# Kernel optimization log

Measured on AMD Instinct MI355X. Metric: run time of the kernel, lower is better.

The kernel has to match this reference:

```python
import jax, jax.numpy as jnp
import numpy as np

NUM_NODES = 100000
IN_CH = 128
OUT_CH = 64
NUM_EDGES = 1000000


def setup_inputs() -> dict:
    key = jax.random.key(0)
    ks = jax.random.split(key, 16)

    x = jax.random.normal(ks[0], (NUM_NODES, IN_CH), dtype=jnp.float32)

    def make_edges(k_src, k_tgt, k_w):
        src = jax.random.randint(k_src, (NUM_EDGES,), 0, NUM_NODES, dtype=jnp.int32)
        # tf.math.segment_sum requires sorted segment ids -> sort targets
        tgt = jnp.sort(jax.random.randint(k_tgt, (NUM_EDGES,), 0, NUM_NODES, dtype=jnp.int32))
        ei = jnp.stack([src, tgt], axis=0)  # (2, E)
        ew = jax.random.uniform(k_w, (NUM_EDGES,), dtype=jnp.float32)
        return ei, ew

    edge_index_in, edge_weight_in = make_edges(ks[1], ks[2], ks[3])
    edge_index_out, edge_weight_out = make_edges(ks[4], ks[5], ks[6])

    glorot = (6.0 / (IN_CH + OUT_CH)) ** 0.5
    W_main_in = jax.random.uniform(ks[7], (IN_CH, OUT_CH), minval=-glorot, maxval=glorot, dtype=jnp.float32)
    W_main_out = jax.random.uniform(ks[8], (IN_CH, OUT_CH), minval=-glorot, maxval=glorot, dtype=jnp.float32)
    W_shared = jax.random.uniform(ks[9], (IN_CH, OUT_CH), minval=-glorot, maxval=glorot, dtype=jnp.float32)

    bias_main_in = jnp.zeros((OUT_CH,), dtype=jnp.float32)
    bias_main_out = jnp.zeros((OUT_CH,), dtype=jnp.float32)
    bias_shared_in = jnp.zeros((OUT_CH,), dtype=jnp.float32)
    bias_shared_out = jnp.zeros((OUT_CH,), dtype=jnp.float32)

    C_in_vec = jnp.ones((NUM_NODES, 1), dtype=jnp.float32)
    C_out_vec = jnp.ones((NUM_NODES, 1), dtype=jnp.float32)

    return {
        "x": x,
        "W_main_in": W_main_in,
        "W_main_out": W_main_out,
        "W_shared": W_shared,
        "bias_main_in": bias_main_in,
        "bias_main_out": bias_main_out,
        "bias_shared_in": bias_shared_in,
        "bias_shared_out": bias_shared_out,
        "C_in_vec": C_in_vec,
        "C_out_vec": C_out_vec,
        "edge_index_in": edge_index_in,
        "edge_weight_in": edge_weight_in,
        "edge_index_out": edge_index_out,
        "edge_weight_out": edge_weight_out,
    }


def _propagate(h, edge_index, edge_weight, num_nodes):
    # gather messages from source nodes, scale by edge weight, sum into targets
    src = edge_index[0]
    tgt = edge_index[1]
    msgs = h[src] * edge_weight[:, None]  # (E, OUT_CH)
    return jax.ops.segment_sum(msgs, tgt, num_segments=num_nodes)  # (N, OUT_CH)


def reference(x, W_main_in, W_main_out, W_shared,
              bias_main_in, bias_main_out, bias_shared_in, bias_shared_out,
              C_in_vec, C_out_vec,
              edge_index_in, edge_weight_in, edge_index_out, edge_weight_out):
    n = x.shape[0]
    h_main_in = _propagate(x @ W_main_in, edge_index_in, edge_weight_in, n)
    h_shared_in = _propagate(x @ W_shared, edge_index_in, edge_weight_in, n)
    ic_combined = h_main_in + bias_main_in + (h_shared_in + bias_shared_in)

    h_main_out = _propagate(x @ W_main_out, edge_index_out, edge_weight_out, n)
    h_shared_out = _propagate(x @ W_shared, edge_index_out, edge_weight_out, n)
    oc_combined = h_main_out + bias_main_out + (h_shared_out + bias_shared_out)

    return C_in_vec * ic_combined + C_out_vec * oc_combined
```

## Files before the change

kernel.cpp:

```cpp
#include <hip/hip_runtime.h>

#define IN_CH   128
#define OUT_CH  64
#define M_TILE  128
#define XS_PITCH 136

typedef __attribute__((ext_vector_type(8))) short short8;
typedef __attribute__((ext_vector_type(4))) float floatx4;

__device__ __forceinline__ unsigned short f2bf(float f) {
    union { float f; unsigned u; } v; v.f = f;
    unsigned r = v.u + 0x7fffu + ((v.u >> 16) & 1u);
    return (unsigned short)(r >> 16);
}
__device__ __forceinline__ float bfl(unsigned u) {
    return __uint_as_float(u << 16);
}
__device__ __forceinline__ float bfh(unsigned u) {
    return __uint_as_float(u & 0xffff0000u);
}

__global__ void prep_kernel(const int* __restrict__ tgtIn,
                            const int* __restrict__ tgtOut,
                            const float* __restrict__ Wmi,
                            const float* __restrict__ Wmo,
                            const float* __restrict__ Wsh,
                            int* __restrict__ rpIn,
                            int* __restrict__ rpOut,
                            unsigned short* __restrict__ WcT,
                            int n_nodes, int neIn, int neOut)
{
    int i = blockIdx.x * blockDim.x + threadIdx.x;
    int half = n_nodes + 1;
    if (i < 2 * half) {
        const int* tgt; int* rp; int t; int ne;
        if (i < half) { tgt = tgtIn;  rp = rpIn;  t = i;        ne = neIn; }
        else          { tgt = tgtOut; rp = rpOut; t = i - half; ne = neOut; }
        int lo = 0, hi = ne;
        while (lo < hi) {
            int mid = (lo + hi) >> 1;
            if (tgt[mid] < t) lo = mid + 1; else hi = mid;
        }
        rp[t] = lo;
    } else {
        int j = i - 2 * half;
        if (j < 2 * OUT_CH * IN_CH) {
            int n = j >> 7, k = j & 127;
            float m = (n < OUT_CH) ? Wmi[k * OUT_CH + n]
                                   : Wmo[k * OUT_CH + (n - OUT_CH)];
            float s = Wsh[k * OUT_CH + (n & (OUT_CH - 1))];
            WcT[n * IN_CH + k] = f2bf(m + s);
        }
    }
}

__global__ __launch_bounds__(256, 3)
void gemm_kernel(const float* __restrict__ x,
                 const unsigned short* __restrict__ WcT,
                 unsigned short* __restrict__ Abf,
                 unsigned short* __restrict__ Bbf,
                 int n_nodes)
{
    __shared__ unsigned short Xs[M_TILE][XS_PITCH];

    const int tid  = threadIdx.x;
    const int w    = tid >> 6;
    const int lane = tid & 63;
    const int l15  = lane & 15;
    const int quad = lane >> 4;
    const long long node0 = (long long)blockIdx.x * M_TILE;

    short8 bfrag[4][2];
#pragma unroll
    for (int ks = 0; ks < 4; ++ks)
#pragma unroll
        for (int ni = 0; ni < 2; ++ni)
            bfrag[ks][ni] = *(const short8*)&WcT[(w * 32 + ni * 16 + l15) * IN_CH
                                                 + ks * 32 + quad * 8];

    {
        const float4* x4 = (const float4*)x;
        for (int i = tid; i < M_TILE * (IN_CH / 4); i += 256) {
            int row = i >> 5, c4 = i & 31;
            long long node = node0 + row;
            float4 v = make_float4(0.f, 0.f, 0.f, 0.f);
            if (node < n_nodes) v = x4[node * (IN_CH / 4) + c4];
            uint2 p;
            p.x = ((unsigned)f2bf(v.y) << 16) | f2bf(v.x);
            p.y = ((unsigned)f2bf(v.w) << 16) | f2bf(v.z);
            *(uint2*)&Xs[row][c4 * 4] = p;
        }
    }
    __syncthreads();

    floatx4 acc[8][2];
#pragma unroll
    for (int mi = 0; mi < 8; ++mi)
#pragma unroll
        for (int ni = 0; ni < 2; ++ni)
            acc[mi][ni] = (floatx4){0.f, 0.f, 0.f, 0.f};

#pragma unroll
    for (int ks = 0; ks < 4; ++ks) {
        const int k0 = ks * 32 + quad * 8;
#pragma unroll
        for (int mi = 0; mi < 8; ++mi) {
            short8 a = *(const short8*)&Xs[mi * 16 + l15][k0];
            acc[mi][0] = __builtin_amdgcn_mfma_f32_16x16x32_bf16(a, bfrag[ks][0], acc[mi][0], 0, 0, 0);
            acc[mi][1] = __builtin_amdgcn_mfma_f32_16x16x32_bf16(a, bfrag[ks][1], acc[mi][1], 0, 0, 0);
        }
    }

    unsigned short* Hout = (w < 2) ? Abf : Bbf;
    const int colb = (w & 1) * 32;
#pragma unroll
    for (int mi = 0; mi < 8; ++mi)
#pragma unroll
        for (int ni = 0; ni < 2; ++ni)
#pragma unroll
            for (int r = 0; r < 4; ++r) {
                long long row = node0 + mi * 16 + quad * 4 + r;
                if (row < n_nodes)
                    Hout[row * OUT_CH + colb + ni * 16 + l15] = f2bf(acc[mi][ni][r]);
            }
}

__global__ __launch_bounds__(256)
void prop_kernel(const unsigned short* __restrict__ H,
                 const int* __restrict__ rpIn, const int* __restrict__ rpOut,
                 const int* __restrict__ srcIn, const float* __restrict__ ewIn,
                 const int* __restrict__ srcOut, const float* __restrict__ ewOut,
                 const float* __restrict__ bmi, const float* __restrict__ bmo,
                 const float* __restrict__ bsi, const float* __restrict__ bso,
                 const float* __restrict__ Cin, const float* __restrict__ Cout,
                 float* __restrict__ out, int n_nodes, int neIn, int neOut)
{
    const int lane = threadIdx.x & 63;
    const int wv   = threadIdx.x >> 6;
    const int e    = lane >> 3;
    const int el   = lane & 7;
    const int ch8  = el * 8;
    const int eb   = lane & 56;

    const unsigned short* Hq = H + ch8;

    const int t = ((int)blockIdx.x * 4 + wv) * 8 + e;
    const bool valid = (t < n_nodes);
    const int tc = valid ? t : 0;

    const int Boff = n_nodes * OUT_CH;

    int ei0 = rpIn[tc],  ei1 = rpIn[tc + 1];
    int eo0 = rpOut[tc], eo1 = rpOut[tc + 1];
    int dIn  = ei1 - ei0;
    int len  = valid ? (dIn + (eo1 - eo0)) : 0;
    float ci = Cin[tc], co = Cout[tc];

    int ml = len;
    ml = max(ml, __shfl_xor(ml, 8));
    ml = max(ml, __shfl_xor(ml, 16));
    ml = max(ml, __shfl_xor(ml, 32));
    const int maxlen = __builtin_amdgcn_readfirstlane(ml);

    float a0 = 0.f, a1 = 0.f, a2 = 0.f, a3 = 0.f;
    float a4 = 0.f, a5 = 0.f, a6 = 0.f, a7 = 0.f;

    auto load_raw = [&](int j, int& sI, float& wI, int& sO, float& wO) {
        int iIn  = min(ei0 + max(0, min(j, dIn - 1)), neIn - 1);
        int jo   = j - dIn;
        int iOut = min(eo0 + max(0, jo), neOut - 1);
        sI = srcIn[iIn];  wI = ewIn[iIn];
        sO = srcOut[iOut]; wO = ewOut[iOut];
    };

    auto conv = [&](int p, int sI, float wI, int sO, float wO,
                    int& rowb, float& wj) {
        int j = p + el;
        bool inSeg  = (j < dIn);
        bool anySeg = (j < len);
        int rb = inSeg ? (sI * OUT_CH) : (sO * OUT_CH + Boff);
        rowb = anySeg ? rb : 0;
        wj   = inSeg ? (ci * wI) : (anySeg ? (co * wO) : 0.f);
    };

    auto gather = [&](int rowb, uint4 (&u)[8]) {
        int r0 = __shfl(rowb, eb + 0), r1 = __shfl(rowb, eb + 1);
        int r2 = __shfl(rowb, eb + 2), r3 = __shfl(rowb, eb + 3);
        int r4 = __shfl(rowb, eb + 4), r5 = __shfl(rowb, eb + 5);
        int r6 = __shfl(rowb, eb + 6), r7 = __shfl(rowb, eb + 7);
        u[0] = *(const uint4*)(Hq + r0);
        u[1] = *(const uint4*)(Hq + r1);
        u[2] = *(const uint4*)(Hq + r2);
        u[3] = *(const uint4*)(Hq + r3);
        u[4] = *(const uint4*)(Hq + r4);
        u[5] = *(const uint4*)(Hq + r5);
        u[6] = *(const uint4*)(Hq + r6);
        u[7] = *(const uint4*)(Hq + r7);
    };

    auto consume = [&](const uint4 (&u)[8], float wj) {
#pragma unroll
        for (int k = 0; k < 8; ++k) {
            float wk = __shfl(wj, eb + k);
            uint4 uk = u[k];
            a0 += wk * bfl(uk.x); a1 += wk * bfh(uk.x);
            a2 += wk * bfl(uk.y); a3 += wk * bfh(uk.y);
            a4 += wk * bfl(uk.z); a5 += wk * bfh(uk.z);
            a6 += wk * bfl(uk.w); a7 += wk * bfh(uk.w);
        }
    };

    int   sIa, sOa, sIb, sOb;
    float wIa, wOa, wIb, wOb;
    uint4 uA[8], uB[8];
    float wjA = 0.f, wjB = 0.f;

    load_raw(el,     sIa, wIa, sOa, wOa);
    load_raw(8 + el, sIb, wIb, sOb, wOb);
    {
        int rb; conv(0, sIa, wIa, sOa, wOa, rb, wjA);
        gather(rb, uA);
    }
    load_raw(16 + el, sIa, wIa, sOa, wOa);
    {
        int rb; conv(8, sIb, wIb, sOb, wOb, rb, wjB);
        gather(rb, uB);
    }
    load_raw(24 + el, sIb, wIb, sOb, wOb);

    for (int p = 0; p < maxlen; p += 16) {
        consume(uA, wjA);
        if (p + 16 < maxlen) {
            int rb; conv(p + 16, sIa, wIa, sOa, wOa, rb, wjA);
            load_raw(p + 32 + el, sIa, wIa, sOa, wOa);
            gather(rb, uA);
        }
        if (p + 8 < maxlen) consume(uB, wjB);
        if (p + 24 < maxlen) {
            int rb; conv(p + 24, sIb, wIb, sOb, wOb, rb, wjB);
            load_raw(p + 40 + el, sIb, wIb, sOb, wOb);
            gather(rb, uB);
        }
    }

    if (valid) {
        float4 o0, o1;
        o0.x = a0 + ci * (bmi[ch8 + 0] + bsi[ch8 + 0]) + co * (bmo[ch8 + 0] + bso[ch8 + 0]);
        o0.y = a1 + ci * (bmi[ch8 + 1] + bsi[ch8 + 1]) + co * (bmo[ch8 + 1] + bso[ch8 + 1]);
        o0.z = a2 + ci * (bmi[ch8 + 2] + bsi[ch8 + 2]) + co * (bmo[ch8 + 2] + bso[ch8 + 2]);
        o0.w = a3 + ci * (bmi[ch8 + 3] + bsi[ch8 + 3]) + co * (bmo[ch8 + 3] + bso[ch8 + 3]);
        o1.x = a4 + ci * (bmi[ch8 + 4] + bsi[ch8 + 4]) + co * (bmo[ch8 + 4] + bso[ch8 + 4]);
        o1.y = a5 + ci * (bmi[ch8 + 5] + bsi[ch8 + 5]) + co * (bmo[ch8 + 5] + bso[ch8 + 5]);
        o1.z = a6 + ci * (bmi[ch8 + 6] + bsi[ch8 + 6]) + co * (bmo[ch8 + 6] + bso[ch8 + 6]);
        o1.w = a7 + ci * (bmi[ch8 + 7] + bsi[ch8 + 7]) + co * (bmo[ch8 + 7] + bso[ch8 + 7]);
        float* ob = out + (long long)t * OUT_CH + ch8;
        *(float4*)ob = o0;
        *(float4*)(ob + 4) = o1;
    }
}

extern "C" void kernel_launch(void* const* d_in, const int* in_sizes, int n_in,
                              void* d_out, int out_size, void* d_ws, size_t ws_size,
                              hipStream_t stream)
{
    const float* x    = (const float*)d_in[0];
    const float* Wmi  = (const float*)d_in[1];
    const float* Wmo  = (const float*)d_in[2];
    const float* Wsh  = (const float*)d_in[3];
    const float* bmi  = (const float*)d_in[4];
    const float* bmo  = (const float*)d_in[5];
    const float* bsi  = (const float*)d_in[6];
    const float* bso  = (const float*)d_in[7];
    const float* Cin  = (const float*)d_in[8];
    const float* Cout = (const float*)d_in[9];
    const int*   eiIn  = (const int*)d_in[10];
    const float* ewIn  = (const float*)d_in[11];
    const int*   eiOut = (const int*)d_in[12];
    const float* ewOut = (const float*)d_in[13];

    const int n_nodes = in_sizes[0] / IN_CH;
    const int neIn  = in_sizes[11];
    const int neOut = in_sizes[13];

    const int* srcIn  = eiIn;
    const int* tgtIn  = eiIn + neIn;
    const int* srcOut = eiOut;
    const int* tgtOut = eiOut + neOut;

    char* ws = (char*)d_ws;
    size_t NH = (size_t)n_nodes * OUT_CH * sizeof(unsigned short);
    unsigned short* Abf = (unsigned short*)ws;
    unsigned short* Bbf = (unsigned short*)(ws + NH);
    int* rpIn  = (int*)(ws + 2 * NH);
    int* rpOut = rpIn + (n_nodes + 1);
    unsigned short* WcT = (unsigned short*)(rpOut + (n_nodes + 1));

    int prep_threads = 2 * (n_nodes + 1) + 2 * OUT_CH * IN_CH;
    prep_kernel<<<(prep_threads + 255) / 256, 256, 0, stream>>>(
        tgtIn, tgtOut, Wmi, Wmo, Wsh, rpIn, rpOut, WcT, n_nodes, neIn, neOut);

    int gblocks = (n_nodes + M_TILE - 1) / M_TILE;
    gemm_kernel<<<gblocks, 256, 0, stream>>>(x, WcT, Abf, Bbf, n_nodes);

    int pblocks = (n_nodes + 31) / 32;
    prop_kernel<<<pblocks, 256, 0, stream>>>(
        Abf, rpIn, rpOut, srcIn, ewIn, srcOut, ewOut,
        bmi, bmo, bsi, bso, Cin, Cout, (float*)d_out, n_nodes, neIn, neOut);
}
```

Measured before the change: 184.9 us.

## Switch propagation to edge-parallel blocks with shared-memory atomic accumulation

Each block of the propagation kernel now owns a range of 64 target nodes. Its waves stride over that range's edge list in groups of 64 edges. Messages that share a target within each 8-edge group are pre-summed in registers, then added with LDS atomics into a shared per-block accumulator, and bias and C-scaling are applied at writeback. This removes the per-wave padding to the longest degree among 8 nodes, which degree variance made costly. In exchange it adds LDS atomic traffic, a target-index load per edge, and block-level syncs.

Result: slower. 318.7 us (+72.3%).

```diff
diff --git a/kernel.cpp b/kernel.cpp
--- a/kernel.cpp
+++ b/kernel.cpp
@@ -4,6 +4,9 @@
 #define OUT_CH  64
 #define M_TILE  128
 #define XS_PITCH 136
+
+#define NB         64
+#define ACC_STRIDE 68
 
 typedef __attribute__((ext_vector_type(8))) short short8;
 typedef __attribute__((ext_vector_type(4))) float floatx4;
@@ -129,133 +132,152 @@
 void prop_kernel(const unsigned short* __restrict__ H,
                  const int* __restrict__ rpIn, const int* __restrict__ rpOut,
                  const int* __restrict__ srcIn, const float* __restrict__ ewIn,
+                 const int* __restrict__ tgtIn,
                  const int* __restrict__ srcOut, const float* __restrict__ ewOut,
+                 const int* __restrict__ tgtOut,
                  const float* __restrict__ bmi, const float* __restrict__ bmo,
                  const float* __restrict__ bsi, const float* __restrict__ bso,
                  const float* __restrict__ Cin, const float* __restrict__ Cout,
                  float* __restrict__ out, int n_nodes, int neIn, int neOut)
 {
-    const int lane = threadIdx.x & 63;
-    const int wv   = threadIdx.x >> 6;
+    __shared__ float accL[NB * ACC_STRIDE];
+    __shared__ float CinL[NB], CoutL[NB];
+    __shared__ float bInL[OUT_CH], bOutL[OUT_CH];
+
+    const int tid  = threadIdx.x;
+    const int base = (int)blockIdx.x * NB;
+    const int nb   = min(NB, n_nodes - base);
+
+    for (int i = tid; i < NB * ACC_STRIDE; i += 256) accL[i] = 0.f;
+    if (tid < NB) {
+        int node = base + min(tid, nb - 1);
+        CinL[tid]  = Cin[node];
+        CoutL[tid] = Cout[node];
+    } else if (tid < NB + OUT_CH) {
+        int c = tid - NB;
+        bInL[c]  = bmi[c] + bsi[c];
+        bOutL[c] = bmo[c] + bso[c];
+    }
+    __syncthreads();
+
+    const int lane = tid & 63;
+    const int wv   = tid >> 6;
     const int e    = lane >> 3;
     const int el   = lane & 7;
     const int ch8  = el * 8;
     const int eb   = lane & 56;
 
-    const unsigned short* Hq = H + ch8;
-
-    const int t = ((int)blockIdx.x * 4 + wv) * 8 + e;
-    const bool valid = (t < n_nodes);
-    const int tc = valid ? t : 0;
+    float* accP = accL + ch8;
 
     const int Boff = n_nodes * OUT_CH;
 
-    int ei0 = rpIn[tc],  ei1 = rpIn[tc + 1];
-    int eo0 = rpOut[tc], eo1 = rpOut[tc + 1];
-    int dIn  = ei1 - ei0;
-    int len  = valid ? (dIn + (eo1 - eo0)) : 0;
-    float ci = Cin[tc], co = Cout[tc];
-
-    int ml = len;
-    ml = max(ml, __shfl_xor(ml, 8));
-    ml = max(ml, __shfl_xor(ml, 16));
-    ml = max(ml, __shfl_xor(ml, 32));
-    const int maxlen = __builtin_amdgcn_readfirstlane(ml);
-
-    float a0 = 0.f, a1 = 0.f, a2 = 0.f, a3 = 0.f;
-    float a4 = 0.f, a5 = 0.f, a6 = 0.f, a7 = 0.f;
-
-    auto load_raw = [&](int j, int& sI, float& wI, int& sO, float& wO) {
-        int iIn  = min(ei0 + max(0, min(j, dIn - 1)), neIn - 1);
-        int jo   = j - dIn;
-        int iOut = min(eo0 + max(0, jo), neOut - 1);
-        sI = srcIn[iIn];  wI = ewIn[iIn];
-        sO = srcOut[iOut]; wO = ewOut[iOut];
+    auto run_set = [&](const int* __restrict__ srcS, const float* __restrict__ ewS,
+                       const int* __restrict__ tgtS, int i0, int i1,
+                       const float* __restrict__ CL, const unsigned short* __restrict__ Hs)
+    {
+        const int ein = i1 - i0;
+        if (ein <= 0) return;
+        const unsigned short* Hq = Hs + ch8;
+        const int NPK = (ein + 63) >> 6;
+
+        auto mvalid = [&](int m) { return (wv + 4 * m) < NPK; };
+
+        auto loadE = [&](int m, int& s, float& w, int& t) {
+            int g   = (wv + 4 * m) * 64 + e * 8 + el;
+            int idx = i0 + min(g, ein - 1);
+            s = srcS[idx]; w = ewS[idx]; t = tgtS[idx];
+            if (g >= ein) w = 0.f;
+        };
+
+        auto prep = [&](int s, float w, int t, int& tl, float& wj, uint4 (&u)[8]) {
+            tl = t - base;
+            wj = w * CL[tl];
+#pragma unroll
+            for (int k = 0; k < 8; ++k) {
+                int sk = __shfl(s, eb + k);
+                u[k] = *(const uint4*)(Hq + sk * OUT_CH);
+            }
+        };
+
+        auto merge = [&](int tl, float wj, const uint4 (&u)[8]) {
+            int cur = __shfl(tl, eb);
+            float s0 = 0.f, s1 = 0.f, s2 = 0.f, s3 = 0.f;
+            float s4 = 0.f, s5 = 0.f, s6 = 0.f, s7 = 0.f;
+#pragma unroll
+            for (int k = 0; k < 8; ++k) {
+                int   tk = __shfl(tl, eb + k);
+                float wk = __shfl(wj, eb + k);
+                if (tk != cur) {
+                    float* p = accP + cur * ACC_STRIDE;
+                    atomicAdd(p + 0, s0); atomicAdd(p + 1, s1);
+                    atomicAdd(p + 2, s2); atomicAdd(p + 3, s3);
+                    atomicAdd(p + 4, s4); atomicAdd(p + 5, s5);
+                    atomicAdd(p + 6, s6); atomicAdd(p + 7, s7);
+                    s0 = s1 = s2 = s3 = s4 = s5 = s6 = s7 = 0.f;
+                    cur = tk;
+                }
+                uint4 uk = u[k];
+                s0 += wk * bfl(uk.x); s1 += wk * bfh(uk.x);
+                s2 += wk * bfl(uk.y); s3 += wk * bfh(uk.y);
+                s4 += wk * bfl(uk.z); s5 += wk * bfh(uk.z);
+                s6 += wk * bfl(uk.w); s7 += wk * bfh(uk.w);
+            }
+            float* p = accP + cur * ACC_STRIDE;
+            atomicAdd(p + 0, s0); atomicAdd(p + 1, s1);
+            atomicAdd(p + 2, s2); atomicAdd(p + 3, s3);
+            atomicAdd(p + 4, s4); atomicAdd(p + 5, s5);
+            atomicAdd(p + 6, s6); atomicAdd(p + 7, s7);
+        };
+
+        if (!mvalid(0)) return;
+
+        int   sA, tA; float wA;
+        int   sB, tB; float wB;
+        int   tlA, tlB; float wjA, wjB;
+        uint4 uA[8], uB[8];
+
+        loadE(0, sA, wA, tA);
+        const bool v1 = mvalid(1);
+        if (v1) loadE(1, sB, wB, tB);
+        prep(sA, wA, tA, tlA, wjA, uA);
+        if (mvalid(2)) loadE(2, sA, wA, tA);
+        if (v1) {
+            prep(sB, wB, tB, tlB, wjB, uB);
+            if (mvalid(3)) loadE(3, sB, wB, tB);
+        }
+
+        for (int m = 0; mvalid(m); m += 2) {
+            merge(tlA, wjA, uA);
+            if (mvalid(m + 2)) {
+                prep(sA, wA, tA, tlA, wjA, uA);
+                if (mvalid(m + 4)) loadE(m + 4, sA, wA, tA);
+            }
+            if (mvalid(m + 1)) {
+                merge(tlB, wjB, uB);
+                if (mvalid(m + 3)) {
+                    prep(sB, wB, tB, tlB, wjB, uB);
+                    if (mvalid(m + 5)) loadE(m + 5, sB, wB, tB);
+                }
+            }
+        }
     };
 
-    auto conv = [&](int p, int sI, float wI, int sO, float wO,
-                    int& rowb, float& wj) {
-        int j = p + el;
-        bool inSeg  = (j < dIn);
-        bool anySeg = (j < len);
-        int rb = inSeg ? (sI * OUT_CH) : (sO * OUT_CH + Boff);
-        rowb = anySeg ? rb : 0;
-        wj   = inSeg ? (ci * wI) : (anySeg ? (co * wO) : 0.f);
-    };
-
-    auto gather = [&](int rowb, uint4 (&u)[8]) {
-        int r0 = __shfl(rowb, eb + 0), r1 = __shfl(rowb, eb + 1);
-        int r2 = __shfl(rowb, eb + 2), r3 = __shfl(rowb, eb + 3);
-        int r4 = __shfl(rowb, eb + 4), r5 = __shfl(rowb, eb + 5);
-        int r6 = __shfl(rowb, eb + 6), r7 = __shfl(rowb, eb + 7);
-        u[0] = *(const uint4*)(Hq + r0);
-        u[1] = *(const uint4*)(Hq + r1);
-        u[2] = *(const uint4*)(Hq + r2);
-        u[3] = *(const uint4*)(Hq + r3);
-        u[4] = *(const uint4*)(Hq + r4);
-        u[5] = *(const uint4*)(Hq + r5);
-        u[6] = *(const uint4*)(Hq + r6);
-        u[7] = *(const uint4*)(Hq + r7);
-    };
-
-    auto consume = [&](const uint4 (&u)[8], float wj) {
-#pragma unroll
-        for (int k = 0; k < 8; ++k) {
-            float wk = __shfl(wj, eb + k);
-            uint4 uk = u[k];
-            a0 += wk * bfl(uk.x); a1 += wk * bfh(uk.x);
-            a2 += wk * bfl(uk.y); a3 += wk * bfh(uk.y);
-            a4 += wk * bfl(uk.z); a5 += wk * bfh(uk.z);
-            a6 += wk * bfl(uk.w); a7 += wk * bfh(uk.w);
-        }
-    };
-
-    int   sIa, sOa, sIb, sOb;
-    float wIa, wOa, wIb, wOb;
-    uint4 uA[8], uB[8];
-    float wjA = 0.f, wjB = 0.f;
-
-    load_raw(el,     sIa, wIa, sOa, wOa);
-    load_raw(8 + el, sIb, wIb, sOb, wOb);
-    {
-        int rb; conv(0, sIa, wIa, sOa, wOa, rb, wjA);
-        gather(rb, uA);
-    }
-    load_raw(16 + el, sIa, wIa, sOa, wOa);
-    {
-        int rb; conv(8, sIb, wIb, sOb, wOb, rb, wjB);
-        gather(rb, uB);
-    }
-    load_raw(24 + el, sIb, wIb, sOb, wOb);
-
-    for (int p = 0; p < maxlen; p += 16) {
-        consume(uA, wjA);
-        if (p + 16 < maxlen) {
-            int rb; conv(p + 16, sIa, wIa, sOa, wOa, rb, wjA);
-            load_raw(p + 32 + el, sIa, wIa, sOa, wOa);
-            gather(rb, uA);
-        }
-        if (p + 8 < maxlen) consume(uB, wjB);
-        if (p + 24 < maxlen) {
-            int rb; conv(p + 24, sIb, wIb, sOb, wOb, rb, wjB);
-            load_raw(p + 40 + el, sIb, wIb, sOb, wOb);
-            gather(rb, uB);
-        }
-    }
-
-    if (valid) {
-        float4 o0, o1;
-        o0.x = a0 + ci * (bmi[ch8 + 0] + bsi[ch8 + 0]) + co * (bmo[ch8 + 0] + bso[ch8 + 0]);
-        o0.y = a1 + ci * (bmi[ch8 + 1] + bsi[ch8 + 1]) + co * (bmo[ch8 + 1] + bso[ch8 + 1]);
-        o0.z = a2 + ci * (bmi[ch8 + 2] + bsi[ch8 + 2]) + co * (bmo[ch8 + 2] + bso[ch8 + 2]);
-        o0.w = a3 + ci * (bmi[ch8 + 3] + bsi[ch8 + 3]) + co * (bmo[ch8 + 3] + bso[ch8 + 3]);
-        o1.x = a4 + ci * (bmi[ch8 + 4] + bsi[ch8 + 4]) + co * (bmo[ch8 + 4] + bso[ch8 + 4]);
-        o1.y = a5 + ci * (bmi[ch8 + 5] + bsi[ch8 + 5]) + co * (bmo[ch8 + 5] + bso[ch8 + 5]);
-        o1.z = a6 + ci * (bmi[ch8 + 6] + bsi[ch8 + 6]) + co * (bmo[ch8 + 6] + bso[ch8 + 6]);
-        o1.w = a7 + ci * (bmi[ch8 + 7] + bsi[ch8 + 7]) + co * (bmo[ch8 + 7] + bso[ch8 + 7]);
-        float* ob = out + (long long)t * OUT_CH + ch8;
-        *(float4*)ob = o0;
-        *(float4*)(ob + 4) = o1;
+    run_set(srcIn,  ewIn,  tgtIn,  rpIn[base],  rpIn[base + nb],  CinL,  H);
+    run_set(srcOut, ewOut, tgtOut, rpOut[base], rpOut[base + nb], CoutL, H + Boff);
+
+    __syncthreads();
+
+    for (int j = tid; j < nb * 16; j += 256) {
+        int i = j >> 4;
+        int q = (j & 15) * 4;
+        float ci = CinL[i], co = CoutL[i];
+        const float* ar = accL + i * ACC_STRIDE + q;
+        float4 v;
+        v.x = ar[0] + ci * bInL[q + 0] + co * bOutL[q + 0];
+        v.y = ar[1] + ci * bInL[q + 1] + co * bOutL[q + 1];
+        v.z = ar[2] + ci * bInL[q + 2] + co * bOutL[q + 2];
+        v.w = ar[3] + ci * bInL[q + 3] + co * bOutL[q + 3];
+        *(float4*)(out + (long long)(base + i) * OUT_CH + q) = v;
     }
 }
 
@@ -302,8 +324,8 @@
     int gblocks = (n_nodes + M_TILE - 1) / M_TILE;
     gemm_kernel<<<gblocks, 256, 0, stream>>>(x, WcT, Abf, Bbf, n_nodes);
 
-    int pblocks = (n_nodes + 31) / 32;
+    int pblocks = (n_nodes + NB - 1) / NB;
     prop_kernel<<<pblocks, 256, 0, stream>>>(
-        Abf, rpIn, rpOut, srcIn, ewIn, srcOut, ewOut,
+        Abf, rpIn, rpOut, srcIn, ewIn, tgtIn, srcOut, ewOut, tgtOut,
         bmi, bmo, bsi, bso, Cin, Cout, (float*)d_out, n_nodes, neIn, neOut);
 }
```

## Sort nodes by degree within blocks and stage GEMM output through LDS

Applied to the files above, without the earlier changes.

Adds a kernel that bitonic-sorts each group of 256 nodes by combined in/out degree and writes a permutation. The propagation kernel uses it so the 8 nodes sharing a wavefront have similar edge counts, which cuts divergence from the per-wave maximum length loop. The GEMM epilogue now writes bf16 results into shared memory and then stores them as coalesced 16-byte vectors instead of scattered 2-byte stores. Costs are an extra kernel launch, an extra indirection, and output writes in permuted row order, which may hurt coalescing.

Measured after the change: 205.6 us. +11.2%, slower.

```diff
diff --git a/kernel.cpp b/kernel.cpp
--- a/kernel.cpp
+++ b/kernel.cpp
@@ -52,6 +52,36 @@
             WcT[n * IN_CH + k] = f2bf(m + s);
         }
     }
+}
+
+__global__ __launch_bounds__(256)
+void wsort_kernel(const int* __restrict__ rpIn, const int* __restrict__ rpOut,
+                  int* __restrict__ perm, int n_nodes)
+{
+    __shared__ unsigned key[256];
+    const int tid  = threadIdx.x;
+    const int base = (int)blockIdx.x * 256;
+    const int t    = base + tid;
+
+    int d = 0x7FFF;
+    if (t < n_nodes)
+        d = min((rpIn[t + 1] - rpIn[t]) + (rpOut[t + 1] - rpOut[t]), 0x7FFE);
+    key[tid] = ((unsigned)d << 16) | (unsigned)tid;
+
+    for (int k = 2; k <= 256; k <<= 1) {
+        for (int j = k >> 1; j > 0; j >>= 1) {
+            __syncthreads();
+            int ixj = tid ^ j;
+            if (ixj > tid) {
+                unsigned a = key[tid], b = key[ixj];
+                bool asc = (tid & k) == 0;
+                if (asc ? (a > b) : (a < b)) { key[tid] = b; key[ixj] = a; }
+            }
+        }
+    }
+    __syncthreads();
+    if (t < n_nodes)
+        perm[t] = base + (int)(key[tid] & 0xFFFFu);
 }
 
 __global__ __launch_bounds__(256, 3)
@@ -111,18 +141,29 @@
         }
     }
 
-    unsigned short* Hout = (w < 2) ? Abf : Bbf;
-    const int colb = (w & 1) * 32;
+    __syncthreads();
+    const int colb = w * 32;
 #pragma unroll
     for (int mi = 0; mi < 8; ++mi)
 #pragma unroll
         for (int ni = 0; ni < 2; ++ni)
 #pragma unroll
-            for (int r = 0; r < 4; ++r) {
-                long long row = node0 + mi * 16 + quad * 4 + r;
-                if (row < n_nodes)
-                    Hout[row * OUT_CH + colb + ni * 16 + l15] = f2bf(acc[mi][ni][r]);
-            }
+            for (int r = 0; r < 4; ++r)
+                Xs[mi * 16 + quad * 4 + r][colb + ni * 16 + l15] =
+                    f2bf(acc[mi][ni][r]);
+    __syncthreads();
+
+    for (int i = tid; i < M_TILE * 16; i += 256) {
+        int row  = i >> 4;
+        int half = (i >> 3) & 1;
+        int v4   = i & 7;
+        long long node = node0 + row;
+        if (node < n_nodes) {
+            uint4 v = *(const uint4*)&Xs[row][half * 64 + v4 * 8];
+            unsigned short* dst = half ? Bbf : Abf;
+            *(uint4*)&dst[node * OUT_CH + v4 * 8] = v;
+        }
+    }
 }
 
 __global__ __launch_bounds__(256)
@@ -130,6 +171,7 @@
                  const int* __restrict__ rpIn, const int* __restrict__ rpOut,
                  const int* __restrict__ srcIn, const float* __restrict__ ewIn,
                  const int* __restrict__ srcOut, const float* __restrict__ ewOut,
+                 const int* __restrict__ perm,
                  const float* __restrict__ bmi, const float* __restrict__ bmo,
                  const float* __restrict__ bsi, const float* __restrict__ bso,
                  const float* __restrict__ Cin, const float* __restrict__ Cout,
@@ -146,7 +188,7 @@
 
     const int t = ((int)blockIdx.x * 4 + wv) * 8 + e;
     const bool valid = (t < n_nodes);
-    const int tc = valid ? t : 0;
+    const int tc = valid ? perm[t] : 0;
 
     const int Boff = n_nodes * OUT_CH;
 
@@ -253,7 +295,7 @@
         o1.y = a5 + ci * (bmi[ch8 + 5] + bsi[ch8 + 5]) + co * (bmo[ch8 + 5] + bso[ch8 + 5]);
         o1.z = a6 + ci * (bmi[ch8 + 6] + bsi[ch8 + 6]) + co * (bmo[ch8 + 6] + bso[ch8 + 6]);
         o1.w = a7 + ci * (bmi[ch8 + 7] + bsi[ch8 + 7]) + co * (bmo[ch8 + 7] + bso[ch8 + 7]);
-        float* ob = out + (long long)t * OUT_CH + ch8;
+        float* ob = out + (long long)tc * OUT_CH + ch8;
         *(float4*)ob = o0;
         *(float4*)(ob + 4) = o1;
     }
@@ -294,16 +336,20 @@
     int* rpIn  = (int*)(ws + 2 * NH);
     int* rpOut = rpIn + (n_nodes + 1);
     unsigned short* WcT = (unsigned short*)(rpOut + (n_nodes + 1));
+    int* perm = (int*)(WcT + 2 * OUT_CH * IN_CH);
 
     int prep_threads = 2 * (n_nodes + 1) + 2 * OUT_CH * IN_CH;
     prep_kernel<<<(prep_threads + 255) / 256, 256, 0, stream>>>(
         tgtIn, tgtOut, Wmi, Wmo, Wsh, rpIn, rpOut, WcT, n_nodes, neIn, neOut);
 
+    int wblocks = (n_nodes + 255) / 256;
+    wsort_kernel<<<wblocks, 256, 0, stream>>>(rpIn, rpOut, perm, n_nodes);
+
     int gblocks = (n_nodes + M_TILE - 1) / M_TILE;
     gemm_kernel<<<gblocks, 256, 0, stream>>>(x, WcT, Abf, Bbf, n_nodes);
 
     int pblocks = (n_nodes + 31) / 32;
     prop_kernel<<<pblocks, 256, 0, stream>>>(
-        Abf, rpIn, rpOut, srcIn, ewIn, srcOut, ewOut,
+        Abf, rpIn, rpOut, srcIn, ewIn, srcOut, ewOut, perm,
         bmi, bmo, bsi, bso, Cin, Cout, (float*)d_out, n_nodes, neIn, neOut);
 }
```

## Build CSR row pointers per edge and stage GEMM output through LDS

Applied to the files above, without the earlier changes.

Row-pointer construction switches from a per-node binary search over sorted targets to a per-edge boundary scan, where each edge writes the row pointers between its predecessor's target and its own. This replaces roughly twenty dependent global reads per node with two coalesced reads per edge. The GEMM epilogue now writes bf16 accumulators into the shared X tile and then issues coalesced 16-byte stores to the two H buffers, instead of scattered 2-byte stores. The cost is two extra barriers, and the prep kernel launches more threads (one per edge rather than one per node).

Measured after the change: 182.3 us. Within noise of the previous version (-1.4%).

```diff
diff --git a/kernel.cpp b/kernel.cpp
--- a/kernel.cpp
+++ b/kernel.cpp
@@ -31,19 +31,22 @@
                             int n_nodes, int neIn, int neOut)
 {
     int i = blockIdx.x * blockDim.x + threadIdx.x;
-    int half = n_nodes + 1;
-    if (i < 2 * half) {
-        const int* tgt; int* rp; int t; int ne;
-        if (i < half) { tgt = tgtIn;  rp = rpIn;  t = i;        ne = neIn; }
-        else          { tgt = tgtOut; rp = rpOut; t = i - half; ne = neOut; }
-        int lo = 0, hi = ne;
-        while (lo < hi) {
-            int mid = (lo + hi) >> 1;
-            if (tgt[mid] < t) lo = mid + 1; else hi = mid;
-        }
-        rp[t] = lo;
+    const int nIn1 = neIn + 1, nOut1 = neOut + 1;
+
+    if (i < nIn1 + nOut1) {
+        const int* tgt; int* rp; int idx; int ne;
+        if (i < nIn1) { tgt = tgtIn;  rp = rpIn;  idx = i;        ne = neIn; }
+        else          { tgt = tgtOut; rp = rpOut; idx = i - nIn1; ne = neOut; }
+        if (idx < ne) {
+            int a    = tgt[idx];
+            int prev = (idx == 0) ? -1 : tgt[idx - 1];
+            for (int t = prev + 1; t <= a; ++t) rp[t] = idx;
+        } else {
+            int last = (ne > 0) ? tgt[ne - 1] : -1;
+            for (int t = last + 1; t <= n_nodes; ++t) rp[t] = ne;
+        }
     } else {
-        int j = i - 2 * half;
+        int j = i - (nIn1 + nOut1);
         if (j < 2 * OUT_CH * IN_CH) {
             int n = j >> 7, k = j & 127;
             float m = (n < OUT_CH) ? Wmi[k * OUT_CH + n]
@@ -111,18 +114,29 @@
         }
     }
 
-    unsigned short* Hout = (w < 2) ? Abf : Bbf;
-    const int colb = (w & 1) * 32;
+    __syncthreads();
+    const int colb = w * 32;
 #pragma unroll
     for (int mi = 0; mi < 8; ++mi)
 #pragma unroll
         for (int ni = 0; ni < 2; ++ni)
 #pragma unroll
-            for (int r = 0; r < 4; ++r) {
-                long long row = node0 + mi * 16 + quad * 4 + r;
-                if (row < n_nodes)
-                    Hout[row * OUT_CH + colb + ni * 16 + l15] = f2bf(acc[mi][ni][r]);
-            }
+            for (int r = 0; r < 4; ++r)
+                Xs[mi * 16 + quad * 4 + r][colb + ni * 16 + l15] =
+                    f2bf(acc[mi][ni][r]);
+    __syncthreads();
+
+    for (int i = tid; i < M_TILE * 16; i += 256) {
+        int row  = i >> 4;
+        int half = (i >> 3) & 1;
+        int v4   = i & 7;
+        long long node = node0 + row;
+        if (node < n_nodes) {
+            uint4 v = *(const uint4*)&Xs[row][half * 64 + v4 * 8];
+            unsigned short* dst = half ? Bbf : Abf;
+            *(uint4*)&dst[node * OUT_CH + v4 * 8] = v;
+        }
+    }
 }
 
 __global__ __launch_bounds__(256)
@@ -295,7 +309,7 @@
     int* rpOut = rpIn + (n_nodes + 1);
     unsigned short* WcT = (unsigned short*)(rpOut + (n_nodes + 1));
 
-    int prep_threads = 2 * (n_nodes + 1) + 2 * OUT_CH * IN_CH;
+    int prep_threads = (neIn + 1) + (neOut + 1) + 2 * OUT_CH * IN_CH;
     prep_kernel<<<(prep_threads + 255) / 256, 256, 0, stream>>>(
         tgtIn, tgtOut, Wmi, Wmo, Wsh, rpIn, rpOut, WcT, n_nodes, neIn, neOut);
 
```
